# Optimization experiments

Measured on AMD Instinct MI355X. Metric: run time of the kernel, lower is better.

## Reference

```python
import jax, jax.numpy as jnp
import numpy as np

N = 50000   # nodes
E = 800000  # edges
F = 128     # input features
W = 128     # hidden width
K = 5       # Chebyshev order


def setup_inputs() -> dict:
    key = jax.random.key(0)
    ks = jax.random.split(key, 12)
    x = jax.random.normal(ks[0], (N, F), jnp.float32)
    edge_index = jax.random.randint(ks[1], (2, E), 0, N, jnp.int32)
    def p(i, shape):
        return jax.random.normal(ks[i], shape, jnp.float32) * 0.05
    return {
        'x': x,
        'edge_index': edge_index,
        'W0': p(2, (K, F, W)), 'b0': p(3, (W,)),
        'W1': p(4, (K, W, W)), 'b1': p(5, (W,)),
        'W2': p(6, (K, W, W)), 'b2': p(7, (W,)),
        'Wl': p(8, (W, 1)),   'bl': p(9, (1,)),
    }


def _norm(edge_index):
    # PyG ChebConv norm with lambda_max=2.0, sym normalization:
    # Lhat = 2/lambda_max * (I - D^-1/2 A D^-1/2) - I  ->  diag 0, offdiag -d_r*d_c
    src, dst = edge_index[0], edge_index[1]
    ew = (src != dst).astype(jnp.float32)  # remove self loops
    deg = jax.ops.segment_sum(ew, src, num_segments=N)
    dinv = jnp.where(deg > 0, jax.lax.rsqrt(jnp.maximum(deg, 1.0)), 0.0)
    w = -ew * dinv[src] * dinv[dst]
    return src, dst, w


def _cheb_conv(h, Wk, b, src, dst, w):
    # Tx_0 = h; Tx_1 = Lhat h; Tx_k = 2 Lhat Tx_{k-1} - Tx_{k-2}
    def matvec(v):
        # gather from src, weight, scatter-add to dst: [E, C] message tensor
        return jax.ops.segment_sum(w[:, None] * v[src], dst, num_segments=N)
    Tx0 = h
    out = Tx0 @ Wk[0]
    Tx1 = matvec(Tx0)
    out = out + Tx1 @ Wk[1]
    for k in range(2, Wk.shape[0]):
        Tx2 = 2.0 * matvec(Tx1) - Tx0
        out = out + Tx2 @ Wk[k]
        Tx0, Tx1 = Tx1, Tx2
    return out + b


def reference(x, edge_index, W0, b0, W1, b1, W2, b2, Wl, bl):
    src, dst, w = _norm(edge_index)
    h = jax.nn.relu(_cheb_conv(x, W0, b0, src, dst, w))  # dropout = identity (eval)
    h = jax.nn.relu(_cheb_conv(h, W1, b1, src, dst, w))
    h = _cheb_conv(h, W2, b2, src, dst, w)
    return h @ Wl + bl  # [N, 1]
```

## Files before the change

kernel.cpp:

```cpp
#include <hip/hip_runtime.h>
#include <hip/hip_bf16.h>
#include <stdint.h>

#define N_NODES 50000
#define N_EDGES 800000
#define FEAT 128
#define CAP 64
#define PSLOT 16
#define NCVT 1600000

#define B_CONV 6250
#define B_TRW  640
#define B_TOT  10018

typedef __attribute__((ext_vector_type(4))) float floatx4;
typedef __attribute__((ext_vector_type(8))) _Float16 half8;
typedef __attribute__((ext_vector_type(4))) _Float16 half4;
typedef __attribute__((ext_vector_type(4))) unsigned short ushortx4;

__device__ __forceinline__ float bf2f(unsigned short u) {
  union { unsigned u; float f; } v; v.u = ((unsigned)u) << 16; return v.f;
}
__device__ __forceinline__ unsigned short f2bf(float f) {
  union { float f; unsigned u; } v; v.f = f;
  unsigned r = v.u + 0x7fffu + ((v.u >> 16) & 1u);
  return (unsigned short)(r >> 16);
}
__device__ __forceinline__ unsigned pack_edge(float w, int s) {
  _Float16 h = (_Float16)w;
  unsigned short hb = __builtin_bit_cast(unsigned short, h);
  return ((unsigned)s << 16) | (unsigned)hb;
}
__device__ __forceinline__ float edge_w(unsigned e) {
  unsigned short hb = (unsigned short)(e & 0xFFFFu);
  return (float)__builtin_bit_cast(_Float16, hb);
}
__device__ __forceinline__ int edge_src(unsigned e) { return (int)(e >> 16); }

__device__ __forceinline__ half8 deq8(uint2 v, float sc) {
  half8 r;
  r[0] = (_Float16)(sc * (float)((int)(v.x & 0xFFu) - 128));
  r[1] = (_Float16)(sc * (float)((int)((v.x >> 8) & 0xFFu) - 128));
  r[2] = (_Float16)(sc * (float)((int)((v.x >> 16) & 0xFFu) - 128));
  r[3] = (_Float16)(sc * (float)((int)(v.x >> 24) - 128));
  r[4] = (_Float16)(sc * (float)((int)(v.y & 0xFFu) - 128));
  r[5] = (_Float16)(sc * (float)((int)((v.y >> 8) & 0xFFu) - 128));
  r[6] = (_Float16)(sc * (float)((int)((v.y >> 16) & 0xFFu) - 128));
  r[7] = (_Float16)(sc * (float)((int)(v.y >> 24) - 128));
  return r;
}

__global__ void k_pre1(const unsigned short* __restrict__ x,
                       const void* b0, const void* b1, const void* b2,
                       const void* wl, const void* bl,
                       float* __restrict__ pf, int* __restrict__ flag) {
  __shared__ int cnt_s;
  __shared__ int fl_s;
  int tid = threadIdx.x;
  if (tid == 0) cnt_s = 0;
  __syncthreads();
  int big = 0;
  for (int i = tid; i < 4096; i += 256) {
    unsigned short u = x[2 * i];
    int e = (u >> 7) & 0xFF;
    if (e >= 0xE0) big++;
  }
  atomicAdd(&cnt_s, big);
  __syncthreads();
  if (tid == 0) { fl_s = (cnt_s > 16) ? 1 : 0; flag[0] = fl_s; }
  __syncthreads();
  int fl = fl_s;
  for (int i = tid; i < 513; i += 256) {
    const void* src; int off;
    if (i < 128)      { src = b0; off = i; }
    else if (i < 256) { src = b1; off = i - 128; }
    else if (i < 384) { src = b2; off = i - 256; }
    else if (i < 512) { src = wl; off = i - 384; }
    else              { src = bl; off = 0; }
    pf[i] = fl ? ((const float*)src)[off] : bf2f(((const unsigned short*)src)[off]);
  }
}

__global__ void k_pre2(const void* __restrict__ xp,
                       const void* __restrict__ w0, const void* __restrict__ w1,
                       const void* __restrict__ w2,
                       const int* __restrict__ esrc, const int* __restrict__ edst,
                       _Float16* __restrict__ t0,
                       unsigned char* __restrict__ q0, float* __restrict__ s0,
                       _Float16* __restrict__ wt,
                       int* __restrict__ deg, int* __restrict__ cnt8,
                       unsigned short* __restrict__ edata16,
                       float* __restrict__ pf,
                       const int* __restrict__ flag) {
  int b = blockIdx.x, tid = threadIdx.x;
  int o;
  if (b < 10000) {
    int g = b >> 4, r = b & 15;
    if (r < 5) {
      int p = b & 7;
      int e = (g * 5 + r) * 256 + tid;
      int s = __builtin_nontemporal_load(esrc + e);
      int d = __builtin_nontemporal_load(edst + e);
      if (s == d) return;
      atomicAdd(&deg[s], 1);
      int pos = atomicAdd(&cnt8[p * N_NODES + d], 1);
      if (pos < PSLOT)
        edata16[(size_t)p * (N_NODES * PSLOT) + d * PSLOT + pos] = (unsigned short)s;
      return;
    }
    o = g * 11 + (r - 5);
  } else {
    o = 6875 + (b - 10000);
  }
  if (o < B_CONV) {
    int i = o * 256 + tid;
    int fl = flag[0];
    floatx4 v;
    if (fl) {
      v = __builtin_nontemporal_load((const floatx4*)xp + i);
    } else {
      ushortx4 u = __builtin_nontemporal_load((const ushortx4*)xp + i);
      v.x = bf2f(u.x); v.y = bf2f(u.y); v.z = bf2f(u.z); v.w = bf2f(u.w);
    }
    half4 h;
    h[0] = (_Float16)v.x; h[1] = (_Float16)v.y; h[2] = (_Float16)v.z; h[3] = (_Float16)v.w;
    ((half4*)t0)[i] = h;
    float mx = fmaxf(fmaxf(fabsf(v.x), fabsf(v.y)), fmaxf(fabsf(v.z), fabsf(v.w)));
#pragma unroll
    for (int d = 1; d < 32; d <<= 1) mx = fmaxf(mx, __shfl_xor(mx, d));
    float inv = mx > 0.f ? 127.f / mx : 0.f;
    int qa = (int)rintf(v.x * inv) + 128;
    int qb = (int)rintf(v.y * inv) + 128;
    int qc = (int)rintf(v.z * inv) + 128;
    int qd = (int)rintf(v.w * inv) + 128;
    ((unsigned*)q0)[i] = (unsigned)qa | ((unsigned)qb << 8) | ((unsigned)qc << 16) | ((unsigned)qd << 24);
    if ((i & 31) == 0) s0[i >> 5] = mx > 0.f ? mx / 127.f : 0.f;
  } else if (o < B_CONV + B_TRW) {
    int t = (o - B_CONV) * 256 + tid;
    int fl = flag[0];
    int li = t >> 14;
    int r = t & 16383;
    int n = r >> 7, kk = r & 127;
    int l = li / 5, k = li - l * 5;
    const void* w = (l == 0) ? w0 : w1;
    int idx = k * 16384 + kk * 128 + n;
    float v = fl ? ((const float*)w)[idx] : bf2f(((const unsigned short*)w)[idx]);
    wt[t] = (_Float16)v;
  } else {
    int t = (o - B_CONV - B_TRW) * 256 + tid;
    if (t > 640) return;
    int fl = flag[0];
    if (t < 640) {
      int k = t >> 7, f = t & 127;
      float s = 0.f;
      const int base = (k << 14) + (f << 7);
      if (fl) {
        const float* w = (const float*)w2 + base;
#pragma unroll 8
        for (int q = 0; q < 128; ++q) s += w[q] * pf[384 + q];
      } else {
        const unsigned short* w = (const unsigned short*)w2 + base;
#pragma unroll 8
        for (int q = 0; q < 128; ++q) s += bf2f(w[q]) * pf[384 + q];
      }
      pf[520 + t] = s;
    } else {
      float s = 0.f;
      for (int q = 0; q < 128; ++q) s += pf[256 + q] * pf[384 + q];
      pf[1160] = s + pf[512];
    }
  }
}

__global__ __launch_bounds__(256) void k_wpack(const unsigned short* __restrict__ ed16,
                                               const int* __restrict__ cnt8,
                                               const int* __restrict__ deg,
                                               int* __restrict__ cnt,
                                               unsigned* __restrict__ edata) {
  int node = (blockIdx.x * 256 + threadIdx.x) >> 6;
  int lane = threadIdx.x & 63;
  if (node >= N_NODES) return;
  int c[8], off[8], tot = 0;
#pragma unroll
  for (int p = 0; p < 8; ++p) {
    int v = cnt8[p * N_NODES + node];
    if (v > PSLOT) v = PSLOT;
    c[p] = v; off[p] = tot; tot += v;
  }
  if (lane == 0) cnt[node] = tot > CAP ? CAP : tot;
  int dd = deg[node];
  float rd = dd > 0 ? rsqrtf((float)dd) : 0.f;
#pragma unroll
  for (int it = 0; it < 2; ++it) {
    int p = (lane >> 4) + it * 4;
    int s = lane & 15;
    if (s < c[p]) {
      int pos = off[p] + s;
      if (pos < CAP) {
        int sr = (int)ed16[(size_t)p * (N_NODES * PSLOT) + node * PSLOT + s];
        int ds = deg[sr];
        float w = (ds > 0 && dd > 0) ? -rsqrtf((float)ds) * rd : 0.f;
        edata[(node << 6) + pos] = pack_edge(w, sr);
      }
    }
  }
}

__global__ __launch_bounds__(256) void k_spmv(const unsigned* __restrict__ edata,
                                              const int* __restrict__ cnt,
                                              const unsigned char* __restrict__ Q,
                                              const float* __restrict__ S,
                                              const _Float16* __restrict__ Z,
                                              _Float16* __restrict__ Y,
                                              unsigned char* __restrict__ Qo,
                                              float* __restrict__ So,
                                              float alpha, int hasZ, int writeY) {
  int wave = threadIdx.x >> 6, lane = threadIdx.x & 63;
  int q = lane >> 4, l16 = lane & 15;
  int node = blockIdx.x * 16 + wave * 4 + q;
  if (node >= N_NODES) return;
  int n_e = cnt[node]; if (n_e > CAP) n_e = CAP;
  int base = node << 6;

  float acc[8];
#pragma unroll
  for (int f = 0; f < 8; ++f) acc[f] = 0.f;
  float wsum = 0.f;

  unsigned e0 = (0 < n_e) ? edata[base + 0] : 0u;
  unsigned e1 = (1 < n_e) ? edata[base + 1] : 0u;
  unsigned e2 = (2 < n_e) ? edata[base + 2] : 0u;
  unsigned e3 = (3 < n_e) ? edata[base + 3] : 0u;
  unsigned e4 = (4 < n_e) ? edata[base + 4] : 0u;
  unsigned e5 = (5 < n_e) ? edata[base + 5] : 0u;
  unsigned e6 = (6 < n_e) ? edata[base + 6] : 0u;
  unsigned e7 = (7 < n_e) ? edata[base + 7] : 0u;
  uint2 r0 = ((const uint2*)(Q + (size_t)edge_src(e0) * FEAT))[l16];
  uint2 r1 = ((const uint2*)(Q + (size_t)edge_src(e1) * FEAT))[l16];
  uint2 r2 = ((const uint2*)(Q + (size_t)edge_src(e2) * FEAT))[l16];
  uint2 r3 = ((const uint2*)(Q + (size_t)edge_src(e3) * FEAT))[l16];
  float s0 = S[edge_src(e0)], s1 = S[edge_src(e1)], s2 = S[edge_src(e2)], s3 = S[edge_src(e3)];

  for (int j = 0; j < n_e; j += 4) {
    float ws0 = edge_w(e0) * s0, ws1 = edge_w(e1) * s1;
    float ws2 = edge_w(e2) * s2, ws3 = edge_w(e3) * s3;
    uint2 c0 = r0, c1 = r1, c2 = r2, c3 = r3;
    e0 = e4; e1 = e5; e2 = e6; e3 = e7;
    e4 = (j + 8 < n_e) ? edata[base + j + 8] : 0u;
    e5 = (j + 9 < n_e) ? edata[base + j + 9] : 0u;
    e6 = (j + 10 < n_e) ? edata[base + j + 10] : 0u;
    e7 = (j + 11 < n_e) ? edata[base + j + 11] : 0u;
    r0 = ((const uint2*)(Q + (size_t)edge_src(e0) * FEAT))[l16];
    r1 = ((const uint2*)(Q + (size_t)edge_src(e1) * FEAT))[l16];
    r2 = ((const uint2*)(Q + (size_t)edge_src(e2) * FEAT))[l16];
    r3 = ((const uint2*)(Q + (size_t)edge_src(e3) * FEAT))[l16];
    s0 = S[edge_src(e0)]; s1 = S[edge_src(e1)]; s2 = S[edge_src(e2)]; s3 = S[edge_src(e3)];
#define DEC8(c, w)                                                        \
    acc[0] = fmaf(w, (float)(c.x & 0xFFu), acc[0]);                       \
    acc[1] = fmaf(w, (float)((c.x >> 8) & 0xFFu), acc[1]);                \
    acc[2] = fmaf(w, (float)((c.x >> 16) & 0xFFu), acc[2]);               \
    acc[3] = fmaf(w, (float)(c.x >> 24), acc[3]);                         \
    acc[4] = fmaf(w, (float)(c.y & 0xFFu), acc[4]);                       \
    acc[5] = fmaf(w, (float)((c.y >> 8) & 0xFFu), acc[5]);                \
    acc[6] = fmaf(w, (float)((c.y >> 16) & 0xFFu), acc[6]);               \
    acc[7] = fmaf(w, (float)(c.y >> 24), acc[7]);
    DEC8(c0, ws0) DEC8(c1, ws1) DEC8(c2, ws2) DEC8(c3, ws3)
#undef DEC8
    wsum += (ws0 + ws1) + (ws2 + ws3);
  }
  float rx[8];
  float b128 = 128.f * wsum;
  if (hasZ) {
    half8 z = ((const half8*)(Z + (size_t)node * FEAT))[l16];
#pragma unroll
    for (int f = 0; f < 8; ++f) rx[f] = fmaf(alpha, acc[f] - b128, -(float)z[f]);
  } else {
#pragma unroll
    for (int f = 0; f < 8; ++f) rx[f] = alpha * (acc[f] - b128);
  }
  if (writeY) {
    half8 res;
#pragma unroll
    for (int f = 0; f < 8; ++f) res[f] = (_Float16)rx[f];
    ((half8*)(Y + (size_t)node * FEAT))[l16] = res;
  }
  float mx = 0.f;
#pragma unroll
  for (int f = 0; f < 8; ++f) mx = fmaxf(mx, fabsf(rx[f]));
#pragma unroll
  for (int o = 1; o < 16; o <<= 1) mx = fmaxf(mx, __shfl_xor(mx, o));
  float inv = mx > 0.f ? 127.f / mx : 0.f;
  int qb[8];
#pragma unroll
  for (int f = 0; f < 8; ++f) qb[f] = (int)rintf(rx[f] * inv) + 128;
  uint2 p;
  p.x = (unsigned)qb[0] | ((unsigned)qb[1] << 8) | ((unsigned)qb[2] << 16) | ((unsigned)qb[3] << 24);
  p.y = (unsigned)qb[4] | ((unsigned)qb[5] << 8) | ((unsigned)qb[6] << 16) | ((unsigned)qb[7] << 24);
  ((uint2*)(Qo + (size_t)node * FEAT))[l16] = p;
  if (l16 == 0) So[node] = mx > 0.f ? mx / 127.f : 0.f;
}

__global__ __launch_bounds__(256) void k_smv(const unsigned* __restrict__ edata,
                                             const int* __restrict__ cnt,
                                             const float* __restrict__ h,
                                             const float* __restrict__ b,
                                             const float* __restrict__ bprev,
                                             float cL, float* __restrict__ y,
                                             int is_out, void* __restrict__ outp,
                                             const int* __restrict__ flag,
                                             const float* __restrict__ cptr) {
  int wave = threadIdx.x >> 6, lane = threadIdx.x & 63;
  int q = lane >> 4, l16 = lane & 15;
  int node = blockIdx.x * 16 + wave * 4 + q;
  if (node >= N_NODES) return;
  int n_e = cnt[node]; if (n_e > CAP) n_e = CAP;
  int base = node << 6;
  float s = 0.f;
  for (int j = l16; j < n_e; j += 16) {
    unsigned e = edata[base + j];
    s = fmaf(edge_w(e), b[edge_src(e)], s);
  }
#pragma unroll
  for (int o = 1; o < 16; o <<= 1) s += __shfl_xor(s, o);
  if (l16 == 0) {
    float r = fmaf(cL, s, h[node]) - (bprev ? bprev[node] : 0.f);
    if (!is_out) {
      y[node] = r;
    } else {
      r += cptr[0];
      if (flag[0]) ((float*)outp)[node] = r;
      else ((unsigned short*)outp)[node] = f2bf(r);
    }
  }
}

__global__ __launch_bounds__(256) void k_gemm(const unsigned char* __restrict__ qa0, const unsigned char* __restrict__ qa1,
                                              const unsigned char* __restrict__ qa2, const unsigned char* __restrict__ qa3,
                                              const unsigned char* __restrict__ qa4,
                                              const float* __restrict__ sa0, const float* __restrict__ sa1,
                                              const float* __restrict__ sa2, const float* __restrict__ sa3,
                                              const float* __restrict__ sa4,
                                              const _Float16* __restrict__ wt,
                                              const float* __restrict__ bias,
                                              _Float16* __restrict__ dst, int mode,
                                              const float* __restrict__ v0,
                                              float* __restrict__ hout,
                                              unsigned char* __restrict__ q8out,
                                              float* __restrict__ scout) {
  __shared__ _Float16 lb[128 * 136];
  const unsigned char* qp[5] = {qa0, qa1, qa2, qa3, qa4};
  const float* sp[5] = {sa0, sa1, sa2, sa3, sa4};
  int tid = threadIdx.x, wave = tid >> 6, lane = tid & 63;
  int quad = lane >> 4, l16 = lane & 15;
  int m0 = blockIdx.x * 128;
  floatx4 acc[2][8];
#pragma unroll
  for (int s = 0; s < 2; ++s)
#pragma unroll
    for (int j = 0; j < 8; ++j) acc[s][j] = (floatx4){0.f, 0.f, 0.f, 0.f};
  int arow[2];
  bool aval[2];
#pragma unroll
  for (int s = 0; s < 2; ++s) {
    arow[s] = m0 + wave * 32 + s * 16 + l16;
    aval[s] = arow[s] < N_NODES;
  }

#pragma unroll
  for (int k = 0; k < 5; ++k) {
    __syncthreads();
    {
      int n = tid >> 1, half = tid & 1;
      const uint4* spw = (const uint4*)(wt + k * 16384 + n * 128 + half * 64);
      uint4* dq = (uint4*)(lb + n * 136 + half * 64);
#pragma unroll
      for (int i = 0; i < 8; ++i) dq[i] = spw[i];
    }
    __syncthreads();
    const unsigned char* Aq = qp[k];
    float sk[2];
#pragma unroll
    for (int s = 0; s < 2; ++s) sk[s] = aval[s] ? sp[k][arow[s]] : 0.f;
#pragma unroll
    for (int ki = 0; ki < 4; ++ki) {
      half8 af[2];
#pragma unroll
      for (int s = 0; s < 2; ++s) {
        uint2 qv = aval[s]
          ? *((const uint2*)(Aq + (size_t)arow[s] * FEAT + ki * 32 + quad * 8))
          : make_uint2(0x80808080u, 0x80808080u);
        af[s] = deq8(qv, sk[s]);
      }
#pragma unroll
      for (int j = 0; j < 8; ++j) {
        half8 bf = *((const half8*)(lb + (j * 16 + l16) * 136 + ki * 32 + quad * 8));
        acc[0][j] = __builtin_amdgcn_mfma_f32_16x16x32_f16(af[0], bf, acc[0][j], 0, 0, 0);
        acc[1][j] = __builtin_amdgcn_mfma_f32_16x16x32_f16(af[1], bf, acc[1][j], 0, 0, 0);
      }
    }
  }
#pragma unroll
  for (int s = 0; s < 2; ++s) {
    int rbase = m0 + wave * 32 + s * 16 + quad * 4;
    if (mode == 0) {
      float mx[4] = {0.f, 0.f, 0.f, 0.f};
#pragma unroll
      for (int j = 0; j < 8; ++j) {
        int col = j * 16 + l16;
        float b = bias[col];
#pragma unroll
        for (int r = 0; r < 4; ++r) {
          int m = rbase + r;
          float v = fmaxf(acc[s][j][r] + b, 0.f);
          if (m < N_NODES) dst[(size_t)m * FEAT + col] = (_Float16)v;
          mx[r] = fmaxf(mx[r], v);
        }
      }
#pragma unroll
      for (int o = 1; o < 16; o <<= 1) {
#pragma unroll
        for (int r = 0; r < 4; ++r) mx[r] = fmaxf(mx[r], __shfl_xor(mx[r], o));
      }
      float inv[4];
#pragma unroll
      for (int r = 0; r < 4; ++r) inv[r] = mx[r] > 0.f ? 127.f / mx[r] : 0.f;
      if (l16 == 0) {
#pragma unroll
        for (int r = 0; r < 4; ++r) {
          int m = rbase + r;
          if (m < N_NODES) scout[m] = mx[r] > 0.f ? mx[r] / 127.f : 0.f;
        }
      }
#pragma unroll
      for (int j = 0; j < 8; ++j) {
        int col = j * 16 + l16;
        float b = bias[col];
#pragma unroll
        for (int r = 0; r < 4; ++r) {
          int m = rbase + r;
          if (m < N_NODES) {
            float v = fmaxf(acc[s][j][r] + b, 0.f);
            int qv = (int)rintf(v * inv[r]) + 128;
            q8out[(size_t)m * FEAT + col] = (unsigned char)qv;
          }
        }
      }
    } else {
      float p[5][4];
#pragma unroll
      for (int k = 0; k < 5; ++k)
#pragma unroll
        for (int r = 0; r < 4; ++r) p[k][r] = 0.f;
#pragma unroll
      for (int j = 0; j < 8; ++j) {
        int col = j * 16 + l16;
        float b = bias[col];
        float vv[5];
#pragma unroll
        for (int k = 0; k < 5; ++k) vv[k] = v0[k * 128 + col];
#pragma unroll
        for (int r = 0; r < 4; ++r) {
          float val = fmaxf(acc[s][j][r] + b, 0.f);
#pragma unroll
          for (int k = 0; k < 5; ++k) p[k][r] = fmaf(val, vv[k], p[k][r]);
        }
      }
#pragma unroll
      for (int o = 1; o < 16; o <<= 1) {
#pragma unroll
        for (int k = 0; k < 5; ++k)
#pragma unroll
          for (int r = 0; r < 4; ++r) p[k][r] += __shfl_xor(p[k][r], o);
      }
      if (l16 == 0) {
#pragma unroll
        for (int r = 0; r < 4; ++r) {
          int m = rbase + r;
          if (m < N_NODES) {
#pragma unroll
            for (int k = 0; k < 5; ++k) hout[k * N_NODES + m] = p[k][r];
          }
        }
      }
    }
  }
}

extern "C" void kernel_launch(void* const* d_in, const int* in_sizes, int n_in,
                              void* d_out, int out_size, void* d_ws, size_t ws_size,
                              hipStream_t stream) {
  const void* x  = d_in[0];
  const int* ei  = (const int*)d_in[1];
  const void* w0 = d_in[2];
  const void* b0 = d_in[3];
  const void* w1 = d_in[4];
  const void* b1 = d_in[5];
  const void* w2 = d_in[6];
  const void* b2 = d_in[7];
  const void* wl = d_in[8];
  const void* bl = d_in[9];
  const int* src = ei;
  const int* dst = ei + N_EDGES;

  char* ws = (char*)d_ws;
  size_t off = 0;
  auto alloc = [&](size_t bytes) -> char* {
    char* p = ws + off;
    off += (bytes + 255) & ~(size_t)255;
    return p;
  };
  _Float16* T[3];
  for (int i = 0; i < 3; ++i) T[i] = (_Float16*)alloc(sizeof(_Float16) * N_NODES * FEAT);
  unsigned char* Q[5];
  for (int i = 0; i < 5; ++i) Q[i] = (unsigned char*)alloc((size_t)N_NODES * FEAT);
  float* S[5];
  for (int i = 0; i < 5; ++i) S[i] = (float*)alloc(sizeof(float) * N_NODES);
  unsigned* edata = (unsigned*)alloc(sizeof(unsigned) * N_NODES * CAP);
  unsigned short* edata16 = (unsigned short*)alloc(sizeof(unsigned short) * 8 * N_NODES * PSLOT);
  int* cnt8 = (int*)alloc(sizeof(int) * N_NODES * 9);
  int* deg = cnt8 + 8 * N_NODES;
  int* cnt = (int*)alloc(sizeof(int) * N_NODES);
  _Float16* wt = (_Float16*)alloc(sizeof(_Float16) * 163840);
  float* pf = (float*)alloc(sizeof(float) * 1536);
  float* hbuf = (float*)alloc(sizeof(float) * 5 * N_NODES);
  float* bbuf = (float*)alloc(sizeof(float) * 3 * N_NODES);
  int* flag = (int*)alloc(sizeof(int));

  hipMemsetAsync(cnt8, 0, sizeof(int) * N_NODES * 9, stream);
  k_pre1<<<1, 256, 0, stream>>>((const unsigned short*)x, b0, b1, b2, wl, bl, pf, flag);
  k_pre2<<<B_TOT, 256, 0, stream>>>(x, w0, w1, w2, src, dst, T[0], Q[0], S[0], wt,
                                    deg, cnt8, edata16, pf, flag);
  k_wpack<<<(N_NODES * 64 + 255) / 256, 256, 0, stream>>>(edata16, cnt8, deg, cnt, edata);

  int nblk_spmv = (N_NODES + 15) / 16;
  int nblk_gemm = (N_NODES + 127) / 128;
  const float* v = pf + 520;
  const float* cc = pf + 1160;

  for (int l = 0; l < 2; ++l) {
    k_spmv<<<nblk_spmv, 256, 0, stream>>>(edata, cnt, Q[0], S[0], nullptr, T[1], Q[1], S[1], 1.f, 0, 1);
    k_spmv<<<nblk_spmv, 256, 0, stream>>>(edata, cnt, Q[1], S[1], T[0], T[2], Q[2], S[2], 2.f, 1, 1);
    k_spmv<<<nblk_spmv, 256, 0, stream>>>(edata, cnt, Q[2], S[2], T[1], nullptr, Q[3], S[3], 2.f, 1, 0);
    k_spmv<<<nblk_spmv, 256, 0, stream>>>(edata, cnt, Q[3], S[3], T[2], nullptr, Q[4], S[4], 2.f, 1, 0);
    k_gemm<<<nblk_gemm, 256, 0, stream>>>(Q[0], Q[1], Q[2], Q[3], Q[4],
                                          S[0], S[1], S[2], S[3], S[4],
                                          wt + l * 5 * 16384, pf + l * 128, T[0],
                                          l, v, hbuf, Q[0], S[0]);
  }
  float* h0 = hbuf;
  float* h1 = hbuf + N_NODES;
  float* h2 = hbuf + 2 * N_NODES;
  float* h3 = hbuf + 3 * N_NODES;
  float* h4 = hbuf + 4 * N_NODES;
  float* b3 = bbuf;
  float* b2c = bbuf + N_NODES;
  float* b1c = bbuf + 2 * N_NODES;
  k_smv<<<nblk_spmv, 256, 0, stream>>>(edata, cnt, h3, h4, nullptr, 2.f, b3, 0, nullptr, flag, nullptr);
  k_smv<<<nblk_spmv, 256, 0, stream>>>(edata, cnt, h2, b3, h4, 2.f, b2c, 0, nullptr, flag, nullptr);
  k_smv<<<nblk_spmv, 256, 0, stream>>>(edata, cnt, h1, b2c, b3, 2.f, b1c, 0, nullptr, flag, nullptr);
  k_smv<<<nblk_spmv, 256, 0, stream>>>(edata, cnt, h0, b1c, b2c, 1.f, nullptr, 1, d_out, flag, cc);
}
```

Baseline: 456.7 us.

## Fuse four scalar Clenshaw SpMV launches into one cooperative grid-synced kernel

Replaces the four back-to-back k_smv launches of the final scalar Clenshaw recurrence with a single cooperative kernel. It uses a grid-stride loop over nodes and grid.sync() between stages, which removes three launch boundaries. The input conversion kernel also switches its T0, Q0 and scale writes to nontemporal stores. The cooperative grid is fixed at 1024 blocks, so work per block rises, and grid-wide barriers cost something of their own.

```diff
diff --git a/kernel.cpp b/kernel.cpp
--- a/kernel.cpp
+++ b/kernel.cpp
@@ -1,6 +1,9 @@
 #include <hip/hip_runtime.h>
 #include <hip/hip_bf16.h>
+#include <hip/hip_cooperative_groups.h>
 #include <stdint.h>
+
+namespace cg = cooperative_groups;
 
 #define N_NODES 50000
 #define N_EDGES 800000
@@ -124,7 +127,7 @@
     }
     half4 h;
     h[0] = (_Float16)v.x; h[1] = (_Float16)v.y; h[2] = (_Float16)v.z; h[3] = (_Float16)v.w;
-    ((half4*)t0)[i] = h;
+    __builtin_nontemporal_store(h, (half4*)t0 + i);
     float mx = fmaxf(fmaxf(fabsf(v.x), fabsf(v.y)), fmaxf(fabsf(v.z), fabsf(v.w)));
 #pragma unroll
     for (int d = 1; d < 32; d <<= 1) mx = fmaxf(mx, __shfl_xor(mx, d));
@@ -133,8 +136,9 @@
     int qb = (int)rintf(v.y * inv) + 128;
     int qc = (int)rintf(v.z * inv) + 128;
     int qd = (int)rintf(v.w * inv) + 128;
-    ((unsigned*)q0)[i] = (unsigned)qa | ((unsigned)qb << 8) | ((unsigned)qc << 16) | ((unsigned)qd << 24);
-    if ((i & 31) == 0) s0[i >> 5] = mx > 0.f ? mx / 127.f : 0.f;
+    unsigned pk = (unsigned)qa | ((unsigned)qb << 8) | ((unsigned)qc << 16) | ((unsigned)qd << 24);
+    __builtin_nontemporal_store(pk, (unsigned*)q0 + i);
+    if ((i & 31) == 0) __builtin_nontemporal_store(mx > 0.f ? mx / 127.f : 0.f, s0 + (i >> 5));
   } else if (o < B_CONV + B_TRW) {
     int t = (o - B_CONV) * 256 + tid;
     int fl = flag[0];
@@ -300,37 +304,60 @@
   if (l16 == 0) So[node] = mx > 0.f ? mx / 127.f : 0.f;
 }
 
-__global__ __launch_bounds__(256) void k_smv(const unsigned* __restrict__ edata,
-                                             const int* __restrict__ cnt,
-                                             const float* __restrict__ h,
-                                             const float* __restrict__ b,
-                                             const float* __restrict__ bprev,
-                                             float cL, float* __restrict__ y,
-                                             int is_out, void* __restrict__ outp,
-                                             const int* __restrict__ flag,
-                                             const float* __restrict__ cptr) {
+__global__ __launch_bounds__(256) void k_clen(const unsigned* __restrict__ edata,
+                                              const int* __restrict__ cnt,
+                                              const float* __restrict__ hb,
+                                              float* __restrict__ bb,
+                                              void* __restrict__ outp,
+                                              const int* __restrict__ flag,
+                                              const float* __restrict__ cptr) {
+  cg::grid_group grid = cg::this_grid();
   int wave = threadIdx.x >> 6, lane = threadIdx.x & 63;
   int q = lane >> 4, l16 = lane & 15;
-  int node = blockIdx.x * 16 + wave * 4 + q;
-  if (node >= N_NODES) return;
-  int n_e = cnt[node]; if (n_e > CAP) n_e = CAP;
-  int base = node << 6;
-  float s = 0.f;
-  for (int j = l16; j < n_e; j += 16) {
-    unsigned e = edata[base + j];
-    s = fmaf(edge_w(e), b[edge_src(e)], s);
-  }
-#pragma unroll
-  for (int o = 1; o < 16; o <<= 1) s += __shfl_xor(s, o);
-  if (l16 == 0) {
-    float r = fmaf(cL, s, h[node]) - (bprev ? bprev[node] : 0.f);
-    if (!is_out) {
-      y[node] = r;
-    } else {
-      r += cptr[0];
-      if (flag[0]) ((float*)outp)[node] = r;
-      else ((unsigned short*)outp)[node] = f2bf(r);
-    }
+  const float* h0 = hb;
+  const float* h1 = hb + N_NODES;
+  const float* h2 = hb + 2 * N_NODES;
+  const float* h3 = hb + 3 * N_NODES;
+  const float* h4 = hb + 4 * N_NODES;
+  float* b3 = bb;
+  float* b2 = bb + N_NODES;
+  float* b1 = bb + 2 * N_NODES;
+  const float* hs[4] = {h3, h2, h1, h0};
+  const float* bs[4] = {h4, b3, b2, b1};
+  const float* ps[4] = {nullptr, h4, b3, b2};
+  float* ys[4] = {b3, b2, b1, nullptr};
+#pragma unroll
+  for (int st = 0; st < 4; ++st) {
+    float cL = (st == 3) ? 1.f : 2.f;
+    const float* bsrc = bs[st];
+    const float* hsrc = hs[st];
+    const float* psrc = ps[st];
+    float* ydst = ys[st];
+    for (int nb = blockIdx.x * 16; nb < N_NODES; nb += gridDim.x * 16) {
+      int node = nb + wave * 4 + q;
+      if (node < N_NODES) {
+        int n_e = cnt[node]; if (n_e > CAP) n_e = CAP;
+        int base = node << 6;
+        float s = 0.f;
+        for (int j = l16; j < n_e; j += 16) {
+          unsigned e = edata[base + j];
+          s = fmaf(edge_w(e), bsrc[edge_src(e)], s);
+        }
+#pragma unroll
+        for (int o = 1; o < 16; o <<= 1) s += __shfl_xor(s, o);
+        if (l16 == 0) {
+          float r = fmaf(cL, s, hsrc[node]) - (psrc ? psrc[node] : 0.f);
+          if (st < 3) {
+            ydst[node] = r;
+          } else {
+            r += cptr[0];
+            if (flag[0]) ((float*)outp)[node] = r;
+            else ((unsigned short*)outp)[node] = f2bf(r);
+          }
+        }
+      }
+    }
+    if (st < 3) grid.sync();
   }
 }
 
@@ -547,16 +574,16 @@
                                           wt + l * 5 * 16384, pf + l * 128, T[0],
                                           l, v, hbuf, Q[0], S[0]);
   }
-  float* h0 = hbuf;
-  float* h1 = hbuf + N_NODES;
-  float* h2 = hbuf + 2 * N_NODES;
-  float* h3 = hbuf + 3 * N_NODES;
-  float* h4 = hbuf + 4 * N_NODES;
-  float* b3 = bbuf;
-  float* b2c = bbuf + N_NODES;
-  float* b1c = bbuf + 2 * N_NODES;
-  k_smv<<<nblk_spmv, 256, 0, stream>>>(edata, cnt, h3, h4, nullptr, 2.f, b3, 0, nullptr, flag, nullptr);
-  k_smv<<<nblk_spmv, 256, 0, stream>>>(edata, cnt, h2, b3, h4, 2.f, b2c, 0, nullptr, flag, nullptr);
-  k_smv<<<nblk_spmv, 256, 0, stream>>>(edata, cnt, h1, b2c, b3, 2.f, b1c, 0, nullptr, flag, nullptr);
-  k_smv<<<nblk_spmv, 256, 0, stream>>>(edata, cnt, h0, b1c, b2c, 1.f, nullptr, 1, d_out, flag, cc);
-}
+  {
+    void* outp = d_out;
+    const unsigned* edc = edata;
+    const int* cntc = cnt;
+    const float* hbc = hbuf;
+    float* bbc = bbuf;
+    const int* flc = flag;
+    const float* ccc = cc;
+    void* args[] = {(void*)&edc, (void*)&cntc, (void*)&hbc, (void*)&bbc,
+                    (void*)&outp, (void*)&flc, (void*)&ccc};
+    hipLaunchCooperativeKernel((const void*)k_clen, dim3(1024), dim3(256), args, 0, stream);
+  }
+}
```

Result: slower. 796.7 us (+74.4%).
